# Kernel tuning notes

Hardware: AMD Instinct MI355X
Metric: run time of the kernel (lower is better)

Reference implementation:

```python
import jax, jax.numpy as jnp
import numpy as np
from jax import lax

T, S = 2000, 100          # trees, nodes per tree
N = T * S                 # total nodes
F = 256                   # in_feats (sent_hidden_size)
H = 256                   # h_feats (prop_hidden_size)


def _build_forest():
    # Random recursive forest: node j in each tree attaches to a uniform earlier node.
    rng = np.random.default_rng(0)
    pl = np.zeros((T, S), np.int64)    # local parent index
    dep = np.zeros((T, S), np.int64)
    rows = np.arange(T)
    for j in range(1, S):
        p = rng.integers(0, j, size=T)
        pl[:, j] = p
        dep[:, j] = dep[rows, p] + 1
    depth = dep.ravel()
    parent = (np.arange(T)[:, None] * S + pl).ravel()
    is_root = (np.arange(N) % S) == 0
    kids = np.arange(N)[~is_root]
    par = parent[~is_root]
    order = np.argsort(par, kind='stable')
    kids_s, par_s = kids[order], par[order]
    counts = np.bincount(par_s, minlength=N)
    C = int(counts.max())
    offsets = np.concatenate([[0], np.cumsum(counts)])
    pos = np.arange(len(kids_s)) - offsets[par_s]
    ch_all = np.full((N, C), N + 1, np.int32)   # pad with dummy zero-hidden row N+1
    ch_all[par_s, pos] = kids_s
    maxd = int(depth.max())
    L = maxd  # processed layers: depths 0..maxd-1 (deepest leaves stay zero, as in torch)
    layer_lists = [np.where(depth == d)[0] for d in range(L)]
    M = max(len(l) for l in layer_lists)
    layer_nodes = np.full((L, M), N, np.int32)  # pad writes to scratch row N
    child_idx = np.full((L, M, C), N + 1, np.int32)
    child_cnt = np.zeros((L, M), np.int32)
    for d, nd in enumerate(layer_lists):
        m = len(nd)
        layer_nodes[d, :m] = nd
        child_idx[d, :m] = ch_all[nd]
        child_cnt[d, :m] = counts[nd]
    root_idx = (np.arange(T) * S).astype(np.int32)
    return layer_nodes, child_idx, child_cnt, root_idx


def setup_inputs() -> dict:
    layer_nodes, child_idx, child_cnt, root_idx = _build_forest()
    key = jax.random.key(0)
    k1, k2, k3, k4, k5 = jax.random.split(key, 5)
    bound = 1.0 / np.sqrt(H)  # torch GRUCell default init
    u = lambda kk, sh: jax.random.uniform(kk, sh, jnp.float32, -bound, bound)
    return {
        'inputs': jax.random.normal(k1, (N, F), jnp.float32),
        'w_ih': u(k2, (3 * H, F)),
        'w_hh': u(k3, (3 * H, H)),
        'b_ih': u(k4, (3 * H,)),
        'b_hh': u(k5, (3 * H,)),
        'layer_nodes': jnp.asarray(layer_nodes),
        'child_idx': jnp.asarray(child_idx),
        'child_cnt': jnp.asarray(child_cnt),
        'root_idx': jnp.asarray(root_idx),
    }


def _gru(x, h, w_ih, w_hh, b_ih, b_hh):
    gi = x @ w_ih.T + b_ih
    gh = h @ w_hh.T + b_hh
    ir, iz, ig = jnp.split(gi, 3, axis=-1)
    hr, hz, hg = jnp.split(gh, 3, axis=-1)
    r = jax.nn.sigmoid(ir + hr)
    z = jax.nn.sigmoid(iz + hz)
    n = jnp.tanh(ig + r * hg)
    return (1.0 - z) * n + z * h


def _forward(inputs, w_ih, w_hh, b_ih, b_hh, layer_nodes, child_idx, child_cnt, root_idx):
    # rows N (scatter scratch for padded slots) and N+1 (always-zero child pad) appended
    x_all = jnp.concatenate([inputs, jnp.zeros((2, F), inputs.dtype)], axis=0)
    h0 = jnp.zeros((N + 2, H), inputs.dtype)

    def step(all_h, layer):
        nodes, cidx, ccnt = layer
        ch = all_h[cidx]                                        # [M, C, H]
        denom = jnp.maximum(ccnt, 1).astype(all_h.dtype)[:, None]
        h_prev = ch.sum(axis=1) / denom                         # mean over children; 0 for leaves
        new_h = _gru(x_all[nodes], h_prev, w_ih, w_hh, b_ih, b_hh)
        return all_h.at[nodes].set(new_h), None

    # process deepest layer first (reversed(range(max_depth)) in the original)
    xs = (layer_nodes[::-1], child_idx[::-1], child_cnt[::-1])
    all_h, _ = lax.scan(step, h0, xs)
    return all_h[root_idx]                                      # [T, H]


def reference(inputs, w_ih, w_hh, b_ih, b_hh, layer_nodes, child_idx, child_cnt, root_idx):
    return _forward(inputs, w_ih, w_hh, b_ih, b_hh, layer_nodes, child_idx, child_cnt, root_idx)
```

## Files before the change

### kernel.cpp

```cpp
#include <hip/hip_runtime.h>
#include <hip/hip_bf16.h>
#include <math.h>

#define N_NODES 200000
#define T_TREES 2000
#define S_NODES 100
#define F_DIM 256
#define H_DIM 256
#define G_DIM 768
#define D_MAX 28

typedef __attribute__((ext_vector_type(8))) short short8b;
typedef __attribute__((ext_vector_type(4))) float f32x4;

static __device__ __forceinline__ unsigned short f2bf(float x) {
    union { __hip_bfloat16 h; unsigned short u; } cv;
    cv.h = __float2bfloat16(x);
    return cv.u;
}
static __device__ __forceinline__ float bf2f(unsigned short u) {
    return __uint_as_float(((unsigned)u) << 16);
}

__global__ void k_zero(float4* __restrict__ p, int n4) {
    float4 z = make_float4(0.f, 0.f, 0.f, 0.f);
    for (int i = blockIdx.x * blockDim.x + threadIdx.x; i < n4;
         i += gridDim.x * blockDim.x)
        p[i] = z;
}

__global__ void k_convx(const float* __restrict__ x, unsigned short* __restrict__ xb,
                        int n8) {
    for (int i = blockIdx.x * blockDim.x + threadIdx.x; i < n8;
         i += gridDim.x * blockDim.x) {
        const float4* px = (const float4*)(x + (size_t)i * 8);
        float4 u = px[0], v = px[1];
        short8b t;
        t[0] = f2bf(u.x); t[1] = f2bf(u.y); t[2] = f2bf(u.z); t[3] = f2bf(u.w);
        t[4] = f2bf(v.x); t[5] = f2bf(v.y); t[6] = f2bf(v.z); t[7] = f2bf(v.w);
        *(short8b*)(xb + (size_t)i * 8) = t;
    }
}

__global__ void k_findM(const int* __restrict__ ln, int LM, int* __restrict__ Mdev) {
    int local = 0x7F7F7F7F;
    for (int p = T_TREES + blockIdx.x * blockDim.x + threadIdx.x; p < LM;
         p += gridDim.x * blockDim.x)
        if (ln[p] < N_NODES && p < local) local = p;
#pragma unroll
    for (int off = 32; off; off >>= 1) {
        int o = __shfl_down(local, off);
        if (o < local) local = o;
    }
    __shared__ int wmin[4];
    if ((threadIdx.x & 63) == 0) wmin[threadIdx.x >> 6] = local;
    __syncthreads();
    if (threadIdx.x == 0) {
        int m = wmin[0];
        for (int i = 1; i < 4; ++i) if (wmin[i] < m) m = wmin[i];
        if (m < 0x7F7F7F7F) atomicMin(Mdev, m);
    }
}

__global__ void k_hist(const int* __restrict__ ln, const int* __restrict__ Mdev,
                       int* __restrict__ layer_cnt, int LM) {
    __shared__ int h[D_MAX];
    if (threadIdx.x < D_MAX) h[threadIdx.x] = 0;
    __syncthreads();
    const int M = Mdev[0];
    for (int p = blockIdx.x * blockDim.x + threadIdx.x; p < LM;
         p += gridDim.x * blockDim.x)
        if (ln[p] < N_NODES) {
            int d = p / M;
            if (d < D_MAX) atomicAdd(&h[d], 1);
        }
    __syncthreads();
    if (threadIdx.x < D_MAX && h[threadIdx.x])
        atomicAdd(&layer_cnt[threadIdx.x], h[threadIdx.x]);
}

__global__ void k_convw(const float* __restrict__ wi, const float* __restrict__ wh,
                        unsigned short* __restrict__ wib, unsigned short* __restrict__ whb) {
    int i = blockIdx.x * blockDim.x + threadIdx.x;
    if (i < G_DIM * F_DIM) {
        wib[i] = f2bf(wi[i]);
        whb[i] = f2bf(wh[i]);
    }
}

__global__ __launch_bounds__(256) void k_gemm_x(
    const unsigned short* __restrict__ xb,
    const unsigned short* __restrict__ wib,
    const float* __restrict__ b_ih,
    unsigned short* __restrict__ gi_all) {
    __shared__ unsigned short Bs[2][64][256];

    const int tid = threadIdx.x;
    const int wv = tid >> 6, lane = tid & 63;
    const int lr = lane & 15, kg = lane >> 4;
    const long m0 = (long)blockIdx.x * 128 + wv * 32;

    short8b A[2][8];
#pragma unroll
    for (int ms = 0; ms < 2; ++ms) {
        long r = m0 + ms * 16 + lr;
        if (r > N_NODES - 1) r = N_NODES - 1;
        const unsigned short* xp = xb + r * F_DIM + kg * 8;
#pragma unroll
        for (int ks = 0; ks < 8; ++ks)
            A[ms][ks] = *(const short8b*)(xp + ks * 32);
    }

    const int sr = tid >> 2, sp = tid & 3;
    const int psr = (sr >> 3) & 1;
    const int gp_off = (lr >> 2) * 8 + (lr & 3);
    const int prow = (gp_off >> 3) & 1;

    short8b st[8];
    {
        const unsigned short* src = wib + (size_t)sr * F_DIM;
#pragma unroll
        for (int q = 0; q < 4; ++q) {
            int c = sp * 16 + q * 64;
            st[2 * q]     = *(const short8b*)(src + c);
            st[2 * q + 1] = *(const short8b*)(src + c + 8);
        }
#pragma unroll
        for (int q = 0; q < 4; ++q) {
            int slot = (sp >> 1) + 2 * q;
            int pc = ((slot ^ psr) << 5) + (sp & 1) * 16;
            *(short8b*)&Bs[0][sr][pc]     = st[2 * q];
            *(short8b*)&Bs[0][sr][pc + 8] = st[2 * q + 1];
        }
    }
    __syncthreads();

    const f32x4 zf = {0.f, 0.f, 0.f, 0.f};

    for (int nt = 0; nt < 12; ++nt) {
        const int cur = nt & 1;
        if (nt < 11) {
            const unsigned short* src = wib + (size_t)((nt + 1) * 64 + sr) * F_DIM;
#pragma unroll
            for (int q = 0; q < 4; ++q) {
                int c = sp * 16 + q * 64;
                st[2 * q]     = *(const short8b*)(src + c);
                st[2 * q + 1] = *(const short8b*)(src + c + 8);
            }
        }
#pragma unroll
        for (int nsp = 0; nsp < 2; ++nsp) {
            f32x4 aP0 = zf, aQ0 = zf, aP1 = zf, aQ1 = zf;
            const int rP = nsp * 32 + gp_off;
#pragma unroll
            for (int ks = 0; ks < 8; ++ks) {
                const int pc = ((ks ^ prow) << 5) + kg * 8;
                short8b BP = *(const short8b*)&Bs[cur][rP][pc];
                short8b BQ = *(const short8b*)&Bs[cur][rP + 4][pc];
                aP0 = __builtin_amdgcn_mfma_f32_16x16x32_bf16(BP, A[0][ks], aP0, 0, 0, 0);
                aQ0 = __builtin_amdgcn_mfma_f32_16x16x32_bf16(BQ, A[0][ks], aQ0, 0, 0, 0);
                aP1 = __builtin_amdgcn_mfma_f32_16x16x32_bf16(BP, A[1][ks], aP1, 0, 0, 0);
                aQ1 = __builtin_amdgcn_mfma_f32_16x16x32_bf16(BQ, A[1][ks], aQ1, 0, 0, 0);
            }
            const int g0 = nt * 64 + nsp * 32 + kg * 8;
            f32x4 b0 = *(const f32x4*)(b_ih + g0);
            f32x4 b1 = *(const f32x4*)(b_ih + g0 + 4);
            long m = m0 + lr;
            if (m < N_NODES) {
                short8b pk;
#pragma unroll
                for (int i = 0; i < 4; ++i) {
                    pk[i]     = f2bf(aP0[i] + b0[i]);
                    pk[4 + i] = f2bf(aQ0[i] + b1[i]);
                }
                *(short8b*)(gi_all + m * G_DIM + g0) = pk;
            }
            m = m0 + 16 + lr;
            if (m < N_NODES) {
                short8b pk;
#pragma unroll
                for (int i = 0; i < 4; ++i) {
                    pk[i]     = f2bf(aP1[i] + b0[i]);
                    pk[4 + i] = f2bf(aQ1[i] + b1[i]);
                }
                *(short8b*)(gi_all + m * G_DIM + g0) = pk;
            }
        }
        if (nt < 11) {
            __syncthreads();
#pragma unroll
            for (int q = 0; q < 4; ++q) {
                int slot = (sp >> 1) + 2 * q;
                int pc = ((slot ^ psr) << 5) + (sp & 1) * 16;
                *(short8b*)&Bs[cur ^ 1][sr][pc]     = st[2 * q];
                *(short8b*)&Bs[cur ^ 1][sr][pc + 8] = st[2 * q + 1];
            }
            __syncthreads();
        }
    }
}

__global__ __launch_bounds__(256) void k_layer(
    const int* __restrict__ layer_nodes,
    const int* __restrict__ child_idx,
    const int* __restrict__ child_cnt,
    const int* __restrict__ Mdev,
    const int* __restrict__ layer_cnt,
    const unsigned short* __restrict__ whb,
    const unsigned short* __restrict__ gi_all,
    const float* __restrict__ b_hh,
    unsigned short* __restrict__ h_all,
    float* __restrict__ out,
    int d, int C) {
    __shared__ unsigned short Ab[32][256];
    __shared__ int Nd[32];

    const int cntd = layer_cnt[d];
    if (cntd == 0) return;
    const int M = Mdev[0];
    const int ntiles = (cntd + 31) >> 5;
    const long pbase = (long)d * M;

    const int tid = threadIdx.x;
    const int wv = tid >> 6, lane = tid & 63;
    const int lr = lane & 15, kg = lane >> 4;
    const int srow = tid >> 3, sc = tid & 7;
    const int psr = (srow >> 3) & 1;
    const int p0 = (lr >> 3) & 1;
    const int prl = (kg >> 1) & 1;

    for (int w = blockIdx.x; w < ntiles * 2; w += gridDim.x) {
        const int tile = w >> 1, cg = w & 1;
        const int cb = cg * 128 + wv * 32;

        __syncthreads();
        {
            int idx = tile * 32 + srow;
            int node = (idx < cntd) ? layer_nodes[pbase + idx] : -1;
            if (sc == 0) Nd[srow] = node;
            int cc = 0;
            const int* ch = nullptr;
            if (node >= 0) {
                cc = child_cnt[pbase + idx];
                ch = child_idx + (size_t)(pbase + idx) * C;
            }
            float inv = 1.0f / (float)(cc > 0 ? cc : 1);
#pragma unroll
            for (int pass = 0; pass < 2; ++pass) {
                const int col = sc * 16 + pass * 128;
                float sum[16];
#pragma unroll
                for (int i = 0; i < 16; ++i) sum[i] = 0.f;
                for (int c = 0; c < cc; ++c) {
                    int kid = ch[c];
                    const unsigned short* hr = h_all + (size_t)kid * H_DIM + col;
                    short8b v0 = *(const short8b*)hr;
                    short8b v1 = *(const short8b*)(hr + 8);
#pragma unroll
                    for (int i = 0; i < 8; ++i) {
                        sum[i]     += bf2f((unsigned short)v0[i]);
                        sum[8 + i] += bf2f((unsigned short)v1[i]);
                    }
                }
                short8b q0, q1;
#pragma unroll
                for (int i = 0; i < 8; ++i) {
                    q0[i] = f2bf(sum[i] * inv);
                    q1[i] = f2bf(sum[8 + i] * inv);
                }
                int slot = (sc >> 1) + pass * 4;
                int pc = ((slot ^ psr) << 5) + (sc & 1) * 16;
                *(short8b*)&Ab[srow][pc]     = q0;
                *(short8b*)&Ab[srow][pc + 8] = q1;
            }
        }
        __syncthreads();

        const f32x4 zf = {0.f, 0.f, 0.f, 0.f};
        f32x4 acc[3][2][2];
#pragma unroll
        for (int c = 0; c < 3; ++c)
#pragma unroll
            for (int ms = 0; ms < 2; ++ms)
#pragma unroll
                for (int ns = 0; ns < 2; ++ns) acc[c][ms][ns] = zf;

#pragma unroll
        for (int ks = 0; ks < 8; ++ks) {
            const int pc = ((ks ^ p0) << 5) + kg * 8;
            short8b A0 = *(const short8b*)&Ab[lr][pc];
            short8b A1 = *(const short8b*)&Ab[16 + lr][pc];
#pragma unroll
            for (int c = 0; c < 3; ++c)
#pragma unroll
                for (int ns = 0; ns < 2; ++ns) {
                    short8b B = *(const short8b*)(whb
                        + (size_t)(c * 256 + cb + ns * 16 + lr) * H_DIM
                        + ks * 32 + kg * 8);
                    acc[c][0][ns] = __builtin_amdgcn_mfma_f32_16x16x32_bf16(
                        A0, B, acc[c][0][ns], 0, 0, 0);
                    acc[c][1][ns] = __builtin_amdgcn_mfma_f32_16x16x32_bf16(
                        A1, B, acc[c][1][ns], 0, 0, 0);
                }
        }

#pragma unroll
        for (int ms = 0; ms < 2; ++ms)
#pragma unroll
            for (int i = 0; i < 4; ++i) {
                const int rl = ms * 16 + kg * 4 + i;
                const int nd = Nd[rl];
                if (nd < 0) continue;
                const unsigned short* gp = gi_all + (size_t)nd * G_DIM;
#pragma unroll
                for (int ns = 0; ns < 2; ++ns) {
                    const int k = cb + ns * 16 + lr;
                    const int hp_pc = (((k >> 5) ^ prl) << 5) + (k & 31);
                    float hp = bf2f(Ab[rl][hp_pc]);
                    float xr = bf2f(gp[k])       + acc[0][ms][ns][i] + b_hh[k];
                    float xz = bf2f(gp[256 + k]) + acc[1][ms][ns][i] + b_hh[256 + k];
                    float r = 1.0f / (1.0f + expf(-xr));
                    float z = 1.0f / (1.0f + expf(-xz));
                    float n = tanhf(bf2f(gp[512 + k]) +
                                    r * (acc[2][ms][ns][i] + b_hh[512 + k]));
                    float h = (1.0f - z) * n + z * hp;
                    if (d == 0) {
                        out[(size_t)(nd / S_NODES) * H_DIM + k] = h;
                    } else {
                        h_all[(size_t)nd * H_DIM + k] = f2bf(h);
                    }
                }
            }
    }
}

extern "C" void kernel_launch(void* const* d_in, const int* in_sizes, int n_in,
                              void* d_out, int out_size, void* d_ws, size_t ws_size,
                              hipStream_t stream) {
    const float* inputs = (const float*)d_in[0];
    const float* w_ih   = (const float*)d_in[1];
    const float* w_hh   = (const float*)d_in[2];
    const float* b_ih   = (const float*)d_in[3];
    const float* b_hh   = (const float*)d_in[4];
    const int* layer_nodes = (const int*)d_in[5];
    const int* child_idx   = (const int*)d_in[6];
    const int* child_cnt   = (const int*)d_in[7];

    const int LM = in_sizes[5];
    const int C  = in_sizes[6] / in_sizes[5];

    char* w = (char*)d_ws;
    size_t o = 0;
    auto alloc = [&](size_t bytes) {
        void* p = w + o;
        o += (bytes + 255) & ~(size_t)255;
        return p;
    };
    unsigned short* wib    = (unsigned short*)alloc((size_t)G_DIM * F_DIM * 2);
    unsigned short* whb    = (unsigned short*)alloc((size_t)G_DIM * H_DIM * 2);
    unsigned short* xb     = (unsigned short*)alloc((size_t)N_NODES * F_DIM * 2);
    unsigned short* h_all  = (unsigned short*)alloc((size_t)N_NODES * H_DIM * 2);
    unsigned short* gi_all = (unsigned short*)alloc((size_t)N_NODES * G_DIM * 2);
    int*            Mdev      = (int*)alloc(4);
    int*            layer_cnt = (int*)alloc(D_MAX * 4);
    (void)ws_size;

    hipMemsetAsync(Mdev, 0x7F, 4, stream);
    hipMemsetAsync(layer_cnt, 0, D_MAX * 4, stream);

    k_zero<<<2048, 256, 0, stream>>>((float4*)h_all, N_NODES * H_DIM * 2 / 16);
    k_convx<<<2048, 256, 0, stream>>>(inputs, xb, N_NODES * F_DIM / 8);
    k_findM<<<256, 256, 0, stream>>>(layer_nodes, LM, Mdev);
    k_hist<<<256, 256, 0, stream>>>(layer_nodes, Mdev, layer_cnt, LM);
    k_convw<<<(G_DIM * F_DIM + 255) / 256, 256, 0, stream>>>(w_ih, w_hh, wib, whb);

    k_gemm_x<<<(N_NODES + 127) / 128, 256, 0, stream>>>(xb, wib, b_ih, gi_all);

    for (int d = D_MAX - 1; d >= 0; --d)
        k_layer<<<1024, 256, 0, stream>>>(layer_nodes, child_idx, child_cnt,
                                          Mdev, layer_cnt, whb, gi_all, b_hh,
                                          h_all, (float*)d_out, d, C);
}
```

Measured before the change: 1.130 ms.

## Process full 256-column tile per 512-thread block and prefetch input gates

Each k_layer block now uses 512 threads (8 waves) to cover all 256 hidden columns of a 32-node tile, instead of splitting columns across two work items. The child-mean gather is therefore done once per tile rather than twice, and its LDS layout uses a new XOR swizzle. The precomputed input-gate values are loaded into registers before the MFMA loop so their latency overlaps the matmul. The trade-off is higher register pressure and a larger launch grid per layer.

```diff
diff --git a/kernel.cpp b/kernel.cpp
--- a/kernel.cpp
+++ b/kernel.cpp
@@ -200,7 +200,7 @@
     }
 }
 
-__global__ __launch_bounds__(256) void k_layer(
+__global__ __launch_bounds__(512) void k_layer(
     const int* __restrict__ layer_nodes,
     const int* __restrict__ child_idx,
     const int* __restrict__ child_cnt,
@@ -224,15 +224,12 @@
     const int tid = threadIdx.x;
     const int wv = tid >> 6, lane = tid & 63;
     const int lr = lane & 15, kg = lane >> 4;
-    const int srow = tid >> 3, sc = tid & 7;
-    const int psr = (srow >> 3) & 1;
-    const int p0 = (lr >> 3) & 1;
-    const int prl = (kg >> 1) & 1;
-
-    for (int w = blockIdx.x; w < ntiles * 2; w += gridDim.x) {
-        const int tile = w >> 1, cg = w & 1;
-        const int cb = cg * 128 + wv * 32;
-
+    const int cb = wv * 32;
+
+    const int srow = tid >> 4;
+    const int sc = tid & 15;
+
+    for (int tile = blockIdx.x; tile < ntiles; tile += gridDim.x) {
         __syncthreads();
         {
             int idx = tile * 32 + srow;
@@ -245,36 +242,50 @@
                 ch = child_idx + (size_t)(pbase + idx) * C;
             }
             float inv = 1.0f / (float)(cc > 0 ? cc : 1);
-#pragma unroll
-            for (int pass = 0; pass < 2; ++pass) {
-                const int col = sc * 16 + pass * 128;
-                float sum[16];
-#pragma unroll
-                for (int i = 0; i < 16; ++i) sum[i] = 0.f;
-                for (int c = 0; c < cc; ++c) {
-                    int kid = ch[c];
-                    const unsigned short* hr = h_all + (size_t)kid * H_DIM + col;
-                    short8b v0 = *(const short8b*)hr;
-                    short8b v1 = *(const short8b*)(hr + 8);
-#pragma unroll
-                    for (int i = 0; i < 8; ++i) {
-                        sum[i]     += bf2f((unsigned short)v0[i]);
-                        sum[8 + i] += bf2f((unsigned short)v1[i]);
-                    }
-                }
-                short8b q0, q1;
+            float sum[16];
+#pragma unroll
+            for (int i = 0; i < 16; ++i) sum[i] = 0.f;
+            for (int c = 0; c < cc; ++c) {
+                int kid = ch[c];
+                const unsigned short* hr = h_all + (size_t)kid * H_DIM + sc * 8;
+                short8b v0 = *(const short8b*)hr;
+                short8b v1 = *(const short8b*)(hr + 128);
 #pragma unroll
                 for (int i = 0; i < 8; ++i) {
-                    q0[i] = f2bf(sum[i] * inv);
-                    q1[i] = f2bf(sum[8 + i] * inv);
-                }
-                int slot = (sc >> 1) + pass * 4;
-                int pc = ((slot ^ psr) << 5) + (sc & 1) * 16;
-                *(short8b*)&Ab[srow][pc]     = q0;
-                *(short8b*)&Ab[srow][pc + 8] = q1;
-            }
+                    sum[i]     += bf2f((unsigned short)v0[i]);
+                    sum[8 + i] += bf2f((unsigned short)v1[i]);
+                }
+            }
+            short8b q0, q1;
+#pragma unroll
+            for (int i = 0; i < 8; ++i) {
+                q0[i] = f2bf(sum[i] * inv);
+                q1[i] = f2bf(sum[8 + i] * inv);
+            }
+            const int g = srow & 7;
+            *(short8b*)&Ab[srow][(sc ^ g) << 3]        = q0;
+            *(short8b*)&Ab[srow][(16 + (sc ^ g)) << 3] = q1;
         }
         __syncthreads();
+
+        int nds[2][4];
+        unsigned short g_r[2][4][2], g_z[2][4][2], g_n[2][4][2];
+#pragma unroll
+        for (int ms = 0; ms < 2; ++ms)
+#pragma unroll
+            for (int i = 0; i < 4; ++i) {
+                int nd = Nd[ms * 16 + kg * 4 + i];
+                nds[ms][i] = nd;
+                const unsigned short* gp =
+                    gi_all + (size_t)(nd >= 0 ? nd : 0) * G_DIM;
+#pragma unroll
+                for (int ns = 0; ns < 2; ++ns) {
+                    int k = cb + ns * 16 + lr;
+                    g_r[ms][i][ns] = gp[k];
+                    g_z[ms][i][ns] = gp[256 + k];
+                    g_n[ms][i][ns] = gp[512 + k];
+                }
+            }
 
         const f32x4 zf = {0.f, 0.f, 0.f, 0.f};
         f32x4 acc[3][2][2];
@@ -287,9 +298,9 @@
 
 #pragma unroll
         for (int ks = 0; ks < 8; ++ks) {
-            const int pc = ((ks ^ p0) << 5) + kg * 8;
-            short8b A0 = *(const short8b*)&Ab[lr][pc];
-            short8b A1 = *(const short8b*)&Ab[16 + lr][pc];
+            const int ch0 = (ks * 4 + kg) ^ (lr & 7);
+            short8b A0 = *(const short8b*)&Ab[lr][ch0 << 3];
+            short8b A1 = *(const short8b*)&Ab[16 + lr][ch0 << 3];
 #pragma unroll
             for (int c = 0; c < 3; ++c)
 #pragma unroll
@@ -309,19 +320,20 @@
 #pragma unroll
             for (int i = 0; i < 4; ++i) {
                 const int rl = ms * 16 + kg * 4 + i;
-                const int nd = Nd[rl];
+                const int nd = nds[ms][i];
                 if (nd < 0) continue;
-                const unsigned short* gp = gi_all + (size_t)nd * G_DIM;
 #pragma unroll
                 for (int ns = 0; ns < 2; ++ns) {
                     const int k = cb + ns * 16 + lr;
-                    const int hp_pc = (((k >> 5) ^ prl) << 5) + (k & 31);
-                    float hp = bf2f(Ab[rl][hp_pc]);
-                    float xr = bf2f(gp[k])       + acc[0][ms][ns][i] + b_hh[k];
-                    float xz = bf2f(gp[256 + k]) + acc[1][ms][ns][i] + b_hh[256 + k];
+                    const int hp_ch = ((k >> 3) ^ (rl & 7)) & 31;
+                    const int hp_off = (((k >> 3) & 24) | (((k >> 3) ^ rl) & 7)) * 8 + (k & 7);
+                    float hp = bf2f(Ab[rl][hp_off]);
+                    (void)hp_ch;
+                    float xr = bf2f(g_r[ms][i][ns]) + acc[0][ms][ns][i] + b_hh[k];
+                    float xz = bf2f(g_z[ms][i][ns]) + acc[1][ms][ns][i] + b_hh[256 + k];
                     float r = 1.0f / (1.0f + expf(-xr));
                     float z = 1.0f / (1.0f + expf(-xz));
-                    float n = tanhf(bf2f(gp[512 + k]) +
+                    float n = tanhf(bf2f(g_n[ms][i][ns]) +
                                     r * (acc[2][ms][ns][i] + b_hh[512 + k]));
                     float h = (1.0f - z) * n + z * hp;
                     if (d == 0) {
@@ -377,7 +389,7 @@
     k_gemm_x<<<(N_NODES + 127) / 128, 256, 0, stream>>>(xb, wib, b_ih, gi_all);
 
     for (int d = D_MAX - 1; d >= 0; --d)
-        k_layer<<<1024, 256, 0, stream>>>(layer_nodes, child_idx, child_cnt,
+        k_layer<<<2048, 512, 0, stream>>>(layer_nodes, child_idx, child_cnt,
                                           Mdev, layer_cnt, whb, gi_all, b_hh,
                                           h_all, (float*)d_out, d, C);
 }
```

New measurement: 1.548 ms. +37.0%, slower.

## Split per-layer work into child-mean gather and LDS-staged recurrent GEMM kernels

Applied to the files above, without the earlier changes.

Each tree layer now runs two kernels. A gather kernel computes the bf16 mean of child hidden states into a dense hprev buffer. A GEMM kernel then multiplies 64-row tiles by W_hh, which is double-buffered through XOR-swizzled shared memory instead of being read straight from global memory. Bias, the gates and the output stores are vectorised, and the exp/tanh calls are replaced with fast rcp/exp approximations. The LDS swizzle in the input GEMM is also changed, and D_MAX drops from 28 to 24, which assumes the forest depth of the test input fits. The cost is twice as many launches, an extra hprev round trip through global memory, and reduced precision from rounding the recurrent gate pre-activations to bf16.

```diff
diff --git a/kernel.cpp b/kernel.cpp
--- a/kernel.cpp
+++ b/kernel.cpp
@@ -8,7 +8,7 @@
 #define F_DIM 256
 #define H_DIM 256
 #define G_DIM 768
-#define D_MAX 28
+#define D_MAX 24
 
 typedef __attribute__((ext_vector_type(8))) short short8b;
 typedef __attribute__((ext_vector_type(4))) float f32x4;
@@ -20,6 +20,12 @@
 }
 static __device__ __forceinline__ float bf2f(unsigned short u) {
     return __uint_as_float(((unsigned)u) << 16);
+}
+static __device__ __forceinline__ float fsig(float x) {
+    return __builtin_amdgcn_rcpf(1.0f + __expf(-x));
+}
+static __device__ __forceinline__ float ftanh(float x) {
+    return 1.0f - 2.0f * __builtin_amdgcn_rcpf(__expf(2.0f * x) + 1.0f);
 }
 
 __global__ void k_zero(float4* __restrict__ p, int n4) {
@@ -112,9 +118,9 @@
     }
 
     const int sr = tid >> 2, sp = tid & 3;
-    const int psr = (sr >> 3) & 1;
+    const int hs = (sr & 3) | (((sr >> 3) & 1) << 2);
     const int gp_off = (lr >> 2) * 8 + (lr & 3);
-    const int prow = (gp_off >> 3) & 1;
+    const int hq = (lr & 3) | (((lr >> 2) & 1) << 2);
 
     short8b st[8];
     {
@@ -127,10 +133,9 @@
         }
 #pragma unroll
         for (int q = 0; q < 4; ++q) {
-            int slot = (sp >> 1) + 2 * q;
-            int pc = ((slot ^ psr) << 5) + (sp & 1) * 16;
-            *(short8b*)&Bs[0][sr][pc]     = st[2 * q];
-            *(short8b*)&Bs[0][sr][pc + 8] = st[2 * q + 1];
+            int c0 = sp * 2 + q * 8, c1 = c0 + 1;
+            *(short8b*)&Bs[0][sr][((c0 & 24) | ((c0 ^ hs) & 7)) << 3] = st[2 * q];
+            *(short8b*)&Bs[0][sr][((c1 & 24) | ((c1 ^ hs) & 7)) << 3] = st[2 * q + 1];
         }
     }
     __syncthreads();
@@ -154,7 +159,8 @@
             const int rP = nsp * 32 + gp_off;
 #pragma unroll
             for (int ks = 0; ks < 8; ++ks) {
-                const int pc = ((ks ^ prow) << 5) + kg * 8;
+                const int c = ks * 4 + kg;
+                const int pc = ((c & 24) | ((c ^ hq) & 7)) << 3;
                 short8b BP = *(const short8b*)&Bs[cur][rP][pc];
                 short8b BQ = *(const short8b*)&Bs[cur][rP + 4][pc];
                 aP0 = __builtin_amdgcn_mfma_f32_16x16x32_bf16(BP, A[0][ks], aP0, 0, 0, 0);
@@ -190,147 +196,220 @@
             __syncthreads();
 #pragma unroll
             for (int q = 0; q < 4; ++q) {
-                int slot = (sp >> 1) + 2 * q;
-                int pc = ((slot ^ psr) << 5) + (sp & 1) * 16;
-                *(short8b*)&Bs[cur ^ 1][sr][pc]     = st[2 * q];
-                *(short8b*)&Bs[cur ^ 1][sr][pc + 8] = st[2 * q + 1];
+                int c0 = sp * 2 + q * 8, c1 = c0 + 1;
+                *(short8b*)&Bs[cur ^ 1][sr][((c0 & 24) | ((c0 ^ hs) & 7)) << 3] = st[2 * q];
+                *(short8b*)&Bs[cur ^ 1][sr][((c1 & 24) | ((c1 ^ hs) & 7)) << 3] = st[2 * q + 1];
             }
             __syncthreads();
         }
     }
 }
 
-__global__ __launch_bounds__(256) void k_layer(
+__global__ void k_gather(
     const int* __restrict__ layer_nodes,
     const int* __restrict__ child_idx,
     const int* __restrict__ child_cnt,
     const int* __restrict__ Mdev,
     const int* __restrict__ layer_cnt,
+    const unsigned short* __restrict__ h_all,
+    unsigned short* __restrict__ hprev,
+    int d, int C) {
+    const int cntd = layer_cnt[d];
+    if (cntd == 0) return;
+    const int M = Mdev[0];
+    const long pbase = (long)d * M;
+    const int total = cntd * 8;
+
+    for (int t = blockIdx.x * blockDim.x + threadIdx.x; t < total;
+         t += gridDim.x * blockDim.x) {
+        const int idx = t >> 3;
+        const int cb = (t & 7) * 32;
+        const int cc = child_cnt[pbase + idx];
+        const int* ch = child_idx + (size_t)(pbase + idx) * C;
+        float sum[32];
+#pragma unroll
+        for (int i = 0; i < 32; ++i) sum[i] = 0.f;
+        for (int c = 0; c < cc; ++c) {
+            const unsigned short* hr = h_all + (size_t)ch[c] * H_DIM + cb;
+#pragma unroll
+            for (int q = 0; q < 4; ++q) {
+                short8b v = *(const short8b*)(hr + q * 8);
+#pragma unroll
+                for (int j = 0; j < 8; ++j)
+                    sum[q * 8 + j] += bf2f((unsigned short)v[j]);
+            }
+        }
+        const float inv = 1.0f / (float)(cc > 0 ? cc : 1);
+        unsigned short* dst = hprev + (size_t)idx * H_DIM + cb;
+#pragma unroll
+        for (int q = 0; q < 4; ++q) {
+            short8b pk;
+#pragma unroll
+            for (int j = 0; j < 8; ++j) pk[j] = f2bf(sum[q * 8 + j] * inv);
+            *(short8b*)(dst + q * 8) = pk;
+        }
+    }
+}
+
+__global__ __launch_bounds__(256, 2) void k_gemm_h(
+    const int* __restrict__ layer_nodes,
+    const int* __restrict__ Mdev,
+    const int* __restrict__ layer_cnt,
     const unsigned short* __restrict__ whb,
+    const unsigned short* __restrict__ hprev,
     const unsigned short* __restrict__ gi_all,
     const float* __restrict__ b_hh,
     unsigned short* __restrict__ h_all,
-    float* __restrict__ out,
-    int d, int C) {
-    __shared__ unsigned short Ab[32][256];
-    __shared__ int Nd[32];
+    float* __restrict__ out, int d) {
+    __shared__ unsigned short Bs[2][64][256];
 
     const int cntd = layer_cnt[d];
     if (cntd == 0) return;
     const int M = Mdev[0];
-    const int ntiles = (cntd + 31) >> 5;
     const long pbase = (long)d * M;
+    const int ntiles = (cntd + 63) >> 6;
 
     const int tid = threadIdx.x;
     const int wv = tid >> 6, lane = tid & 63;
     const int lr = lane & 15, kg = lane >> 4;
-    const int srow = tid >> 3, sc = tid & 7;
-    const int psr = (srow >> 3) & 1;
-    const int p0 = (lr >> 3) & 1;
-    const int prl = (kg >> 1) & 1;
-
-    for (int w = blockIdx.x; w < ntiles * 2; w += gridDim.x) {
-        const int tile = w >> 1, cg = w & 1;
-        const int cb = cg * 128 + wv * 32;
+
+    const int sr = tid >> 2, sp = tid & 3;
+    const int hs = (sr & 3) | (((sr >> 3) & 1) << 2);
+    const int gp_off = (lr >> 2) * 8 + (lr & 3);
+    const int hq = (lr & 3) | (((lr >> 2) & 1) << 2);
+
+    for (int tile = blockIdx.x; tile < ntiles; tile += gridDim.x) {
+        const int m0 = tile * 64 + wv * 16;
+        int r = m0 + lr;
+        const bool valid = r < cntd;
+        if (r > cntd - 1) r = cntd - 1;
+
+        short8b A[8];
+        {
+            const unsigned short* hp = hprev + (size_t)r * H_DIM + kg * 8;
+#pragma unroll
+            for (int ks = 0; ks < 8; ++ks)
+                A[ks] = *(const short8b*)(hp + ks * 32);
+        }
 
         __syncthreads();
         {
-            int idx = tile * 32 + srow;
-            int node = (idx < cntd) ? layer_nodes[pbase + idx] : -1;
-            if (sc == 0) Nd[srow] = node;
-            int cc = 0;
-            const int* ch = nullptr;
-            if (node >= 0) {
-                cc = child_cnt[pbase + idx];
-                ch = child_idx + (size_t)(pbase + idx) * C;
-            }
-            float inv = 1.0f / (float)(cc > 0 ? cc : 1);
-#pragma unroll
-            for (int pass = 0; pass < 2; ++pass) {
-                const int col = sc * 16 + pass * 128;
-                float sum[16];
-#pragma unroll
-                for (int i = 0; i < 16; ++i) sum[i] = 0.f;
-                for (int c = 0; c < cc; ++c) {
-                    int kid = ch[c];
-                    const unsigned short* hr = h_all + (size_t)kid * H_DIM + col;
-                    short8b v0 = *(const short8b*)hr;
-                    short8b v1 = *(const short8b*)(hr + 8);
-#pragma unroll
-                    for (int i = 0; i < 8; ++i) {
-                        sum[i]     += bf2f((unsigned short)v0[i]);
-                        sum[8 + i] += bf2f((unsigned short)v1[i]);
+            const unsigned short* src = whb + (size_t)sr * H_DIM;
+            short8b s0[8];
+#pragma unroll
+            for (int q = 0; q < 4; ++q) {
+                int c = sp * 16 + q * 64;
+                s0[2 * q]     = *(const short8b*)(src + c);
+                s0[2 * q + 1] = *(const short8b*)(src + c + 8);
+            }
+#pragma unroll
+            for (int q = 0; q < 4; ++q) {
+                int c0 = sp * 2 + q * 8, c1 = c0 + 1;
+                *(short8b*)&Bs[0][sr][((c0 & 24) | ((c0 ^ hs) & 7)) << 3] = s0[2 * q];
+                *(short8b*)&Bs[0][sr][((c1 & 24) | ((c1 ^ hs) & 7)) << 3] = s0[2 * q + 1];
+            }
+        }
+        __syncthreads();
+
+        short8b ghp[12][2];
+        short8b st[8];
+        const f32x4 zf = {0.f, 0.f, 0.f, 0.f};
+
+#pragma unroll
+        for (int nt = 0; nt < 12; ++nt) {
+            const int cur = nt & 1;
+            if (nt < 11) {
+                const unsigned short* src = whb + (size_t)((nt + 1) * 64 + sr) * H_DIM;
+#pragma unroll
+                for (int q = 0; q < 4; ++q) {
+                    int c = sp * 16 + q * 64;
+                    st[2 * q]     = *(const short8b*)(src + c);
+                    st[2 * q + 1] = *(const short8b*)(src + c + 8);
+                }
+            }
+#pragma unroll
+            for (int nsp = 0; nsp < 2; ++nsp) {
+                f32x4 aP = zf, aQ = zf;
+                const int rP = nsp * 32 + gp_off;
+#pragma unroll
+                for (int ks = 0; ks < 8; ++ks) {
+                    const int c = ks * 4 + kg;
+                    const int pc = ((c & 24) | ((c ^ hq) & 7)) << 3;
+                    short8b BP = *(const short8b*)&Bs[cur][rP][pc];
+                    short8b BQ = *(const short8b*)&Bs[cur][rP + 4][pc];
+                    aP = __builtin_amdgcn_mfma_f32_16x16x32_bf16(BP, A[ks], aP, 0, 0, 0);
+                    aQ = __builtin_amdgcn_mfma_f32_16x16x32_bf16(BQ, A[ks], aQ, 0, 0, 0);
+                }
+                short8b pk;
+#pragma unroll
+                for (int i = 0; i < 4; ++i) {
+                    pk[i]     = f2bf(aP[i]);
+                    pk[4 + i] = f2bf(aQ[i]);
+                }
+                ghp[nt][nsp] = pk;
+            }
+            if (nt < 11) {
+                __syncthreads();
+#pragma unroll
+                for (int q = 0; q < 4; ++q) {
+                    int c0 = sp * 2 + q * 8, c1 = c0 + 1;
+                    *(short8b*)&Bs[cur ^ 1][sr][((c0 & 24) | ((c0 ^ hs) & 7)) << 3] = st[2 * q];
+                    *(short8b*)&Bs[cur ^ 1][sr][((c1 & 24) | ((c1 ^ hs) & 7)) << 3] = st[2 * q + 1];
+                }
+                __syncthreads();
+            }
+        }
+
+        if (valid) {
+            const int nd = layer_nodes[pbase + m0 + lr];
+            const unsigned short* gp = gi_all + (size_t)nd * G_DIM;
+            const unsigned short* hpr = hprev + (size_t)r * H_DIM;
+#pragma unroll
+            for (int q = 0; q < 4; ++q)
+#pragma unroll
+                for (int nsp = 0; nsp < 2; ++nsp) {
+                    const int k = q * 64 + nsp * 32 + kg * 8;
+                    short8b gir = *(const short8b*)(gp + k);
+                    short8b giz = *(const short8b*)(gp + 256 + k);
+                    short8b gin = *(const short8b*)(gp + 512 + k);
+                    short8b hpv = *(const short8b*)(hpr + k);
+                    f32x4 br0 = *(const f32x4*)(b_hh + k);
+                    f32x4 br1 = *(const f32x4*)(b_hh + k + 4);
+                    f32x4 bz0 = *(const f32x4*)(b_hh + 256 + k);
+                    f32x4 bz1 = *(const f32x4*)(b_hh + 256 + k + 4);
+                    f32x4 bn0 = *(const f32x4*)(b_hh + 512 + k);
+                    f32x4 bn1 = *(const f32x4*)(b_hh + 512 + k + 4);
+                    short8b ghr = ghp[q][nsp];
+                    short8b ghz = ghp[q + 4][nsp];
+                    short8b ghn = ghp[q + 8][nsp];
+                    float hv[8];
+#pragma unroll
+                    for (int j = 0; j < 8; ++j) {
+                        float bhr = (j < 4) ? br0[j] : br1[j - 4];
+                        float bhz = (j < 4) ? bz0[j] : bz1[j - 4];
+                        float bhn = (j < 4) ? bn0[j] : bn1[j - 4];
+                        float xr = bf2f((unsigned short)gir[j]) +
+                                   bf2f((unsigned short)ghr[j]) + bhr;
+                        float xz = bf2f((unsigned short)giz[j]) +
+                                   bf2f((unsigned short)ghz[j]) + bhz;
+                        float rr = fsig(xr);
+                        float zz = fsig(xz);
+                        float nn = ftanh(bf2f((unsigned short)gin[j]) +
+                                         rr * (bf2f((unsigned short)ghn[j]) + bhn));
+                        hv[j] = (1.0f - zz) * nn + zz * bf2f((unsigned short)hpv[j]);
                     }
-                }
-                short8b q0, q1;
-#pragma unroll
-                for (int i = 0; i < 8; ++i) {
-                    q0[i] = f2bf(sum[i] * inv);
-                    q1[i] = f2bf(sum[8 + i] * inv);
-                }
-                int slot = (sc >> 1) + pass * 4;
-                int pc = ((slot ^ psr) << 5) + (sc & 1) * 16;
-                *(short8b*)&Ab[srow][pc]     = q0;
-                *(short8b*)&Ab[srow][pc + 8] = q1;
-            }
-        }
-        __syncthreads();
-
-        const f32x4 zf = {0.f, 0.f, 0.f, 0.f};
-        f32x4 acc[3][2][2];
-#pragma unroll
-        for (int c = 0; c < 3; ++c)
-#pragma unroll
-            for (int ms = 0; ms < 2; ++ms)
-#pragma unroll
-                for (int ns = 0; ns < 2; ++ns) acc[c][ms][ns] = zf;
-
-#pragma unroll
-        for (int ks = 0; ks < 8; ++ks) {
-            const int pc = ((ks ^ p0) << 5) + kg * 8;
-            short8b A0 = *(const short8b*)&Ab[lr][pc];
-            short8b A1 = *(const short8b*)&Ab[16 + lr][pc];
-#pragma unroll
-            for (int c = 0; c < 3; ++c)
-#pragma unroll
-                for (int ns = 0; ns < 2; ++ns) {
-                    short8b B = *(const short8b*)(whb
-                        + (size_t)(c * 256 + cb + ns * 16 + lr) * H_DIM
-                        + ks * 32 + kg * 8);
-                    acc[c][0][ns] = __builtin_amdgcn_mfma_f32_16x16x32_bf16(
-                        A0, B, acc[c][0][ns], 0, 0, 0);
-                    acc[c][1][ns] = __builtin_amdgcn_mfma_f32_16x16x32_bf16(
-                        A1, B, acc[c][1][ns], 0, 0, 0);
-                }
-        }
-
-#pragma unroll
-        for (int ms = 0; ms < 2; ++ms)
-#pragma unroll
-            for (int i = 0; i < 4; ++i) {
-                const int rl = ms * 16 + kg * 4 + i;
-                const int nd = Nd[rl];
-                if (nd < 0) continue;
-                const unsigned short* gp = gi_all + (size_t)nd * G_DIM;
-#pragma unroll
-                for (int ns = 0; ns < 2; ++ns) {
-                    const int k = cb + ns * 16 + lr;
-                    const int hp_pc = (((k >> 5) ^ prl) << 5) + (k & 31);
-                    float hp = bf2f(Ab[rl][hp_pc]);
-                    float xr = bf2f(gp[k])       + acc[0][ms][ns][i] + b_hh[k];
-                    float xz = bf2f(gp[256 + k]) + acc[1][ms][ns][i] + b_hh[256 + k];
-                    float r = 1.0f / (1.0f + expf(-xr));
-                    float z = 1.0f / (1.0f + expf(-xz));
-                    float n = tanhf(bf2f(gp[512 + k]) +
-                                    r * (acc[2][ms][ns][i] + b_hh[512 + k]));
-                    float h = (1.0f - z) * n + z * hp;
                     if (d == 0) {
-                        out[(size_t)(nd / S_NODES) * H_DIM + k] = h;
+                        float* op = out + (size_t)(nd / S_NODES) * H_DIM + k;
+                        *(float4*)op = make_float4(hv[0], hv[1], hv[2], hv[3]);
+                        *(float4*)(op + 4) = make_float4(hv[4], hv[5], hv[6], hv[7]);
                     } else {
-                        h_all[(size_t)nd * H_DIM + k] = f2bf(h);
+                        short8b ph;
+#pragma unroll
+                        for (int j = 0; j < 8; ++j) ph[j] = f2bf(hv[j]);
+                        *(short8b*)(h_all + (size_t)nd * H_DIM + k) = ph;
                     }
                 }
-            }
+        }
     }
 }
 
@@ -360,6 +439,7 @@
     unsigned short* whb    = (unsigned short*)alloc((size_t)G_DIM * H_DIM * 2);
     unsigned short* xb     = (unsigned short*)alloc((size_t)N_NODES * F_DIM * 2);
     unsigned short* h_all  = (unsigned short*)alloc((size_t)N_NODES * H_DIM * 2);
+    unsigned short* hprev  = (unsigned short*)alloc((size_t)N_NODES * H_DIM * 2);
     unsigned short* gi_all = (unsigned short*)alloc((size_t)N_NODES * G_DIM * 2);
     int*            Mdev      = (int*)alloc(4);
     int*            layer_cnt = (int*)alloc(D_MAX * 4);
@@ -376,8 +456,11 @@
 
     k_gemm_x<<<(N_NODES + 127) / 128, 256, 0, stream>>>(xb, wib, b_ih, gi_all);
 
-    for (int d = D_MAX - 1; d >= 0; --d)
-        k_layer<<<1024, 256, 0, stream>>>(layer_nodes, child_idx, child_cnt,
-                                          Mdev, layer_cnt, whb, gi_all, b_hh,
-                                          h_all, (float*)d_out, d, C);
-}
+    for (int d = D_MAX - 1; d >= 0; --d) {
+        k_gather<<<1024, 256, 0, stream>>>(layer_nodes, child_idx, child_cnt,
+                                           Mdev, layer_cnt, h_all, hprev, d, C);
+        k_gemm_h<<<1024, 256, 0, stream>>>(layer_nodes, Mdev, layer_cnt,
+                                           whb, hprev, gi_all, b_hh,
+                                           h_all, (float*)d_out, d);
+    }
+}
```

After: 2.004 ms. 77.3% more time.
